# Optimization experiments

Measured on AMD Instinct MI355X. Metric: run time of the kernel, lower is better.

## Reference

```python
import jax, jax.numpy as jnp
import numpy as np

LENGTH_MIN = 5
LENGTH_MAX = 64
EMBED_DIM = 512
POOL_SIZE = 20
TOP_K = 5
BETA = 0.5
LN_EPS = 1e-5
COS_EPS = 1e-8


def setup_inputs() -> dict:
    key = jax.random.key(0)
    ks = jax.random.split(key, 8)
    B, N = 1024, 64
    H = EMBED_DIM // 2
    # xavier-uniform-ish init scale for params
    def xavier(k, shape, fan_in, fan_out):
        lim = float(np.sqrt(6.0 / (fan_in + fan_out)))
        return jax.random.uniform(k, shape, jnp.float32, -lim, lim)
    return {
        "x_embed": jax.random.normal(ks[0], (B, N, EMBED_DIM), jnp.float32),
        "quality_score": jax.random.uniform(ks[1], (B, 1), jnp.float32),
        "prompt_keys": xavier(ks[2], (POOL_SIZE, EMBED_DIM), POOL_SIZE, EMBED_DIM),
        "prompt_embeddings": xavier(ks[3], (POOL_SIZE, LENGTH_MAX, EMBED_DIM), LENGTH_MAX, EMBED_DIM),
        "w1": xavier(ks[4], (1, H), 1, H),
        "b1": jnp.zeros((H,), jnp.float32),
        "ln_g": jnp.ones((H,), jnp.float32),
        "ln_b": jnp.zeros((H,), jnp.float32),
        "w2": xavier(ks[5], (H, EMBED_DIM), H, EMBED_DIM),
        "b2": jnp.zeros((EMBED_DIM,), jnp.float32),
    }


def _quality_proj(q, w1, b1, ln_g, ln_b, w2, b2):
    h = q @ w1 + b1  # [B, H]
    mu = h.mean(-1, keepdims=True)
    var = ((h - mu) ** 2).mean(-1, keepdims=True)
    h = (h - mu) * jax.lax.rsqrt(var + LN_EPS) * ln_g + ln_b
    h = jax.nn.relu(h)
    return h @ w2 + b2  # [B, D]


def reference(x_embed, quality_score, prompt_keys, prompt_embeddings, w1, b1, ln_g, ln_b, w2, b2):
    query = _quality_proj(quality_score, w1, b1, ln_g, ln_b, w2, b2)  # [B, D]
    # cosine similarity vs pool keys
    qn = query / jnp.maximum(jnp.linalg.norm(query, axis=-1, keepdims=True), COS_EPS)
    kn = prompt_keys / jnp.maximum(jnp.linalg.norm(prompt_keys, axis=-1, keepdims=True), COS_EPS)
    sims = qn @ kn.T  # [B, P]
    scale = 1.0 + BETA * quality_score.mean()
    weights = jax.nn.softmax(sims * scale, axis=1)  # [B, P]
    # batched top-k (replaces the per-sample Python loop)
    topk_w, topk_idx = jax.lax.top_k(weights, TOP_K)  # [B, K]
    # per-sample dynamic length -> validity mask over length_max positions
    mu_b = quality_score.mean(axis=1)  # [B]; quality_score[b:b+1].mean()
    len_f = LENGTH_MIN + (LENGTH_MAX - LENGTH_MIN) * (1.0 - mu_b / 5.0)
    lens = jnp.clip(jnp.trunc(len_f).astype(jnp.int32), LENGTH_MIN, LENGTH_MAX)  # [B]
    mask = (jnp.arange(LENGTH_MAX)[None, :] < lens[:, None]).astype(x_embed.dtype)  # [B, L]
    # gather selected prompts and weighted-sum over top_k
    sel = prompt_embeddings[topk_idx]  # [B, K, L, D]
    out = jnp.einsum("bk,bkld->bld", topk_w, sel) * mask[:, :, None]  # [B, L, D]
    return out
```

## Files before the change

kernel.cpp:

```cpp
#include <hip/hip_runtime.h>
#include <hip/hip_bf16.h>
#include <math.h>

#define LENGTH_MIN 5
#define LENGTH_MAX 64
#define EMBED_DIM 512
#define HDIM      256
#define POOL      20
#define TOPK      5
#define BETA      0.5f
#define LN_EPS    1e-5f
#define COS_EPS   1e-8f


__device__ __forceinline__ float blockReduceSum(float v, float* red) {
    int t = threadIdx.x;
    red[t] = v;
    __syncthreads();
    for (int off = 128; off > 0; off >>= 1) {
        if (t < off) red[t] += red[t + off];
        __syncthreads();
    }
    float r = red[0];
    __syncthreads();
    return r;
}

__global__ __launch_bounds__(256) void prep_kernel(
    const float* __restrict__ quality, const float* __restrict__ keys,
    const float* __restrict__ w1, const float* __restrict__ b1,
    float* __restrict__ ws, int B)
{
    __shared__ float red[256];
    int t = threadIdx.x;
    int blk = blockIdx.x;
    if (blk == 0) {
        float s = 0.f;
        for (int i = t; i < B; i += 256) s += quality[i];
        float tot = blockReduceSum(s, red);
        if (t == 0) ws[0] = tot / (float)B;
    } else if (blk == 1) {
        float a = w1[t];
        float c = b1[t];
        float mw1 = blockReduceSum(a, red) / 256.f;
        float mb1 = blockReduceSum(c, red) / 256.f;
        float da = a - mw1, dc = c - mb1;
        float Vw1 = blockReduceSum(da * da, red) / 256.f;
        float Vb1 = blockReduceSum(dc * dc, red) / 256.f;
        float Cv  = blockReduceSum(da * dc, red) / 256.f;
        if (t == 0) { ws[1] = mw1; ws[2] = mb1; ws[3] = Vw1; ws[4] = Vb1; ws[5] = Cv; }
    } else {
        int p = blk - 2;
        const float* kp = keys + p * EMBED_DIM;
        float s = 0.f;
        float x0 = kp[t], x1 = kp[t + 256];
        s = x0 * x0 + x1 * x1;
        float n2 = blockReduceSum(s, red);
        if (t == 0) ws[8 + p] = 1.f / fmaxf(sqrtf(n2), COS_EPS);
    }
}

__global__ __launch_bounds__(256) void query_kernel(
    const float* __restrict__ quality, const float* __restrict__ keys,
    const float* __restrict__ w1, const float* __restrict__ b1,
    const float* __restrict__ ln_g, const float* __restrict__ ln_b,
    const float* __restrict__ w2, const float* __restrict__ b2,
    float* __restrict__ ws, int B)
{
    __shared__ float hn_s[4][HDIM];
    __shared__ float qbuf[4][EMBED_DIM];
    int t = threadIdx.x;
    int b0 = blockIdx.x * 4;

    float qmean = ws[0];
    float mw1 = ws[1], mb1 = ws[2], Vw1 = ws[3], Vb1 = ws[4], Cv = ws[5];
    float invk[POOL];
    #pragma unroll
    for (int p = 0; p < POOL; p++) invk[p] = ws[8 + p];

    float w1t = w1[t], b1t = b1[t], gt = ln_g[t], lbt = ln_b[t];
    float qv4[4];
    #pragma unroll
    for (int bi = 0; bi < 4; bi++) {
        float q = quality[b0 + bi];
        qv4[bi] = q;
        float mu  = q * mw1 + mb1;
        float var = q * q * Vw1 + 2.f * q * Cv + Vb1;
        float inv = rsqrtf(var + LN_EPS);
        float h = q * w1t + b1t;
        float v = (h - mu) * inv * gt + lbt;
        hn_s[bi][t] = fmaxf(v, 0.f);
    }
    __syncthreads();

    int d0 = 2 * t;
    float2 b2v = *(const float2*)(b2 + d0);
    float acc0[4], acc1[4];
    #pragma unroll
    for (int bi = 0; bi < 4; bi++) { acc0[bi] = b2v.x; acc1[bi] = b2v.y; }

    for (int j = 0; j < HDIM; j += 4) {
        float2 wv0 = *(const float2*)(w2 + (j + 0) * EMBED_DIM + d0);
        float2 wv1 = *(const float2*)(w2 + (j + 1) * EMBED_DIM + d0);
        float2 wv2 = *(const float2*)(w2 + (j + 2) * EMBED_DIM + d0);
        float2 wv3 = *(const float2*)(w2 + (j + 3) * EMBED_DIM + d0);
        #pragma unroll
        for (int bi = 0; bi < 4; bi++) {
            float4 hv = *(const float4*)&hn_s[bi][j];
            acc0[bi] = fmaf(hv.x, wv0.x, acc0[bi]);
            acc1[bi] = fmaf(hv.x, wv0.y, acc1[bi]);
            acc0[bi] = fmaf(hv.y, wv1.x, acc0[bi]);
            acc1[bi] = fmaf(hv.y, wv1.y, acc1[bi]);
            acc0[bi] = fmaf(hv.z, wv2.x, acc0[bi]);
            acc1[bi] = fmaf(hv.z, wv2.y, acc1[bi]);
            acc0[bi] = fmaf(hv.w, wv3.x, acc0[bi]);
            acc1[bi] = fmaf(hv.w, wv3.y, acc1[bi]);
        }
    }
    #pragma unroll
    for (int bi = 0; bi < 4; bi++) {
        *(float2*)&qbuf[bi][d0] = make_float2(acc0[bi], acc1[bi]);
    }
    __syncthreads();

    int wave = t >> 6, lane = t & 63;
    int bi = wave;
    float s[POOL + 1];
    #pragma unroll
    for (int p = 0; p <= POOL; p++) s[p] = 0.f;
    #pragma unroll
    for (int i = 0; i < 8; i++) {
        int d = lane + 64 * i;
        float qd = qbuf[bi][d];
        s[POOL] = fmaf(qd, qd, s[POOL]);
        #pragma unroll
        for (int p = 0; p < POOL; p++)
            s[p] = fmaf(qd, keys[p * EMBED_DIM + d], s[p]);
    }
    #pragma unroll
    for (int off = 32; off > 0; off >>= 1) {
        #pragma unroll
        for (int p = 0; p <= POOL; p++) s[p] += __shfl_xor(s[p], off);
    }

    float invq = 1.f / fmaxf(sqrtf(s[POOL]), COS_EPS);
    float scale = 1.f + BETA * qmean;
    float sim[POOL];
    #pragma unroll
    for (int p = 0; p < POOL; p++) sim[p] = s[p] * invq * invk[p] * scale;

    float m = sim[0];
    #pragma unroll
    for (int p = 1; p < POOL; p++) m = fmaxf(m, sim[p]);
    float e[POOL]; float den = 0.f;
    #pragma unroll
    for (int p = 0; p < POOL; p++) { e[p] = __expf(sim[p] - m); den += e[p]; }
    den = 0.f;
    #pragma unroll
    for (int p = 0; p < POOL; p++) { e[p] = expf(sim[p] - m); den += e[p]; }
    float invden = 1.f / den;

    unsigned picked = 0;
    float tw[TOPK]; int ti[TOPK];
    #pragma unroll
    for (int k = 0; k < TOPK; k++) {
        float best = -1.f; int bidx = 0;
        #pragma unroll
        for (int p = 0; p < POOL; p++) {
            bool free_p = ((picked >> p) & 1u) == 0u;
            if (free_p && e[p] > best) { best = e[p]; bidx = p; }
        }
        picked |= (1u << bidx);
        tw[k] = best * invden;
        ti[k] = bidx;
    }

    if (lane == 0) {
        int b = b0 + bi;
        float* topw = ws + 32;
        int*   topi = (int*)(ws + 32) + 5 * B;
        int*   lenp = (int*)(ws + 32) + 10 * B;
        #pragma unroll
        for (int k = 0; k < TOPK; k++) {
            topw[b * TOPK + k] = tw[k];
            topi[b * TOPK + k] = ti[k];
        }
        float q = qv4[bi];
        float lf = __fadd_rn(5.f, __fmul_rn(59.f, __fsub_rn(1.f, __fdiv_rn(q, 5.f))));
        int len = (int)truncf(lf);
        len = min(max(len, LENGTH_MIN), LENGTH_MAX);
        lenp[b] = len;
    }
}

__global__ __launch_bounds__(256) void scatter_kernel(
    const float* __restrict__ pe, const float* __restrict__ ws,
    float* __restrict__ out, int B)
{
    int b  = blockIdx.x >> 3;
    int l0 = (blockIdx.x & 7) * 8;
    const float* topw = ws + 32;
    const int*   topi = (const int*)(ws + 32) + 5 * B;
    const int*   lenp = (const int*)(ws + 32) + 10 * B;

    float w[TOPK]; int idx[TOPK];
    #pragma unroll
    for (int k = 0; k < TOPK; k++) {
        w[k]   = topw[b * TOPK + k];
        idx[k] = topi[b * TOPK + k];
    }
    int len = lenp[b];

    int t = threadIdx.x;
    #pragma unroll
    for (int sweep = 0; sweep < 4; sweep++) {
        int l  = l0 + sweep * 2 + (t >> 7);
        int d4 = (t & 127) * 4;
        float4 r = make_float4(0.f, 0.f, 0.f, 0.f);
        if (l < len) {
            #pragma unroll
            for (int k = 0; k < TOPK; k++) {
                const float4 pv = *(const float4*)(pe + (idx[k] * 64 + l) * EMBED_DIM + d4);
                r.x = fmaf(w[k], pv.x, r.x);
                r.y = fmaf(w[k], pv.y, r.y);
                r.z = fmaf(w[k], pv.z, r.z);
                r.w = fmaf(w[k], pv.w, r.w);
            }
        }
        *(float4*)(out + ((size_t)(b * 64 + l)) * EMBED_DIM + d4) = r;
    }
}

extern "C" void kernel_launch(void* const* d_in, const int* in_sizes, int n_in,
                              void* d_out, int out_size, void* d_ws, size_t ws_size,
                              hipStream_t stream) {
    const float* quality = (const float*)d_in[1];
    const float* keys    = (const float*)d_in[2];
    const float* pe      = (const float*)d_in[3];
    const float* w1      = (const float*)d_in[4];
    const float* b1      = (const float*)d_in[5];
    const float* ln_g    = (const float*)d_in[6];
    const float* ln_b    = (const float*)d_in[7];
    const float* w2      = (const float*)d_in[8];
    const float* b2      = (const float*)d_in[9];
    float* out = (float*)d_out;
    float* ws  = (float*)d_ws;
    int B = in_sizes[1];

    prep_kernel<<<2 + POOL, 256, 0, stream>>>(quality, keys, w1, b1, ws, B);
    query_kernel<<<B / 4, 256, 0, stream>>>(quality, keys, w1, b1, ln_g, ln_b, w2, b2, ws, B);
    scatter_kernel<<<B * 8, 256, 0, stream>>>(pe, ws, out, B);
}
```

Measured before the change: 294.9 us.

## Fold prep stats into query kernel and use nontemporal output stores

```diff
diff --git a/kernel.cpp b/kernel.cpp
--- a/kernel.cpp
+++ b/kernel.cpp
@@ -12,73 +12,60 @@
 #define LN_EPS    1e-5f
 #define COS_EPS   1e-8f
 
-
-__device__ __forceinline__ float blockReduceSum(float v, float* red) {
-    int t = threadIdx.x;
-    red[t] = v;
-    __syncthreads();
-    for (int off = 128; off > 0; off >>= 1) {
-        if (t < off) red[t] += red[t + off];
-        __syncthreads();
-    }
-    float r = red[0];
-    __syncthreads();
-    return r;
-}
-
-__global__ __launch_bounds__(256) void prep_kernel(
-    const float* __restrict__ quality, const float* __restrict__ keys,
-    const float* __restrict__ w1, const float* __restrict__ b1,
-    float* __restrict__ ws, int B)
-{
-    __shared__ float red[256];
-    int t = threadIdx.x;
-    int blk = blockIdx.x;
-    if (blk == 0) {
-        float s = 0.f;
-        for (int i = t; i < B; i += 256) s += quality[i];
-        float tot = blockReduceSum(s, red);
-        if (t == 0) ws[0] = tot / (float)B;
-    } else if (blk == 1) {
-        float a = w1[t];
-        float c = b1[t];
-        float mw1 = blockReduceSum(a, red) / 256.f;
-        float mb1 = blockReduceSum(c, red) / 256.f;
-        float da = a - mw1, dc = c - mb1;
-        float Vw1 = blockReduceSum(da * da, red) / 256.f;
-        float Vb1 = blockReduceSum(dc * dc, red) / 256.f;
-        float Cv  = blockReduceSum(da * dc, red) / 256.f;
-        if (t == 0) { ws[1] = mw1; ws[2] = mb1; ws[3] = Vw1; ws[4] = Vb1; ws[5] = Cv; }
-    } else {
-        int p = blk - 2;
-        const float* kp = keys + p * EMBED_DIM;
-        float s = 0.f;
-        float x0 = kp[t], x1 = kp[t + 256];
-        s = x0 * x0 + x1 * x1;
-        float n2 = blockReduceSum(s, red);
-        if (t == 0) ws[8 + p] = 1.f / fmaxf(sqrtf(n2), COS_EPS);
-    }
-}
-
-__global__ __launch_bounds__(256) void query_kernel(
+typedef float v4f __attribute__((ext_vector_type(4)));
+
+
+__global__ __launch_bounds__(256) void query_all_kernel(
     const float* __restrict__ quality, const float* __restrict__ keys,
     const float* __restrict__ w1, const float* __restrict__ b1,
     const float* __restrict__ ln_g, const float* __restrict__ ln_b,
     const float* __restrict__ w2, const float* __restrict__ b2,
     float* __restrict__ ws, int B)
 {
+    __shared__ float red[24];
+    __shared__ float invk_s[POOL];
     __shared__ float hn_s[4][HDIM];
     __shared__ float qbuf[4][EMBED_DIM];
+
     int t = threadIdx.x;
+    int wave = t >> 6, lane = t & 63;
     int b0 = blockIdx.x * 4;
 
-    float qmean = ws[0];
-    float mw1 = ws[1], mb1 = ws[2], Vw1 = ws[3], Vb1 = ws[4], Cv = ws[5];
-    float invk[POOL];
-    #pragma unroll
-    for (int p = 0; p < POOL; p++) invk[p] = ws[8 + p];
-
-    float w1t = w1[t], b1t = b1[t], gt = ln_g[t], lbt = ln_b[t];
+    float qpart = 0.f;
+    for (int i = t; i < B; i += 256) qpart += quality[i];
+    float a = w1[t], c = b1[t];
+    float vals[6] = { qpart, a, a * a, c, c * c, a * c };
+    #pragma unroll
+    for (int i = 0; i < 6; i++) {
+        float v = vals[i];
+        #pragma unroll
+        for (int off = 32; off > 0; off >>= 1) v += __shfl_xor(v, off);
+        if (lane == 0) red[i * 4 + wave] = v;
+    }
+    #pragma unroll
+    for (int j = 0; j < 5; j++) {
+        int p = wave + 4 * j;
+        const float* kp = keys + p * EMBED_DIM;
+        float s = 0.f;
+        #pragma unroll
+        for (int i = 0; i < 8; i++) { float x = kp[lane + 64 * i]; s = fmaf(x, x, s); }
+        #pragma unroll
+        for (int off = 32; off > 0; off >>= 1) s += __shfl_xor(s, off);
+        if (lane == 0) invk_s[p] = 1.f / fmaxf(sqrtf(s), COS_EPS);
+    }
+    __syncthreads();
+
+    float qmean = (red[0] + red[1] + red[2] + red[3]) / (float)B;
+    float mw1   = (red[4] + red[5] + red[6] + red[7]) * (1.f / 256.f);
+    float Ew2   = (red[8] + red[9] + red[10] + red[11]) * (1.f / 256.f);
+    float mb1   = (red[12] + red[13] + red[14] + red[15]) * (1.f / 256.f);
+    float Eb2   = (red[16] + red[17] + red[18] + red[19]) * (1.f / 256.f);
+    float Eab   = (red[20] + red[21] + red[22] + red[23]) * (1.f / 256.f);
+    float Vw1 = Ew2 - mw1 * mw1;
+    float Vb1 = Eb2 - mb1 * mb1;
+    float Cv  = Eab - mw1 * mb1;
+
+    float gt = ln_g[t], lbt = ln_b[t];
     float qv4[4];
     #pragma unroll
     for (int bi = 0; bi < 4; bi++) {
@@ -87,9 +74,8 @@
         float mu  = q * mw1 + mb1;
         float var = q * q * Vw1 + 2.f * q * Cv + Vb1;
         float inv = rsqrtf(var + LN_EPS);
-        float h = q * w1t + b1t;
-        float v = (h - mu) * inv * gt + lbt;
-        hn_s[bi][t] = fmaxf(v, 0.f);
+        float h = q * a + c;
+        hn_s[bi][t] = fmaxf((h - mu) * inv * gt + lbt, 0.f);
     }
     __syncthreads();
 
@@ -118,12 +104,10 @@
         }
     }
     #pragma unroll
-    for (int bi = 0; bi < 4; bi++) {
+    for (int bi = 0; bi < 4; bi++)
         *(float2*)&qbuf[bi][d0] = make_float2(acc0[bi], acc1[bi]);
-    }
     __syncthreads();
 
-    int wave = t >> 6, lane = t & 63;
     int bi = wave;
     float s[POOL + 1];
     #pragma unroll
@@ -143,19 +127,16 @@
         for (int p = 0; p <= POOL; p++) s[p] += __shfl_xor(s[p], off);
     }
 
-    float invq = 1.f / fmaxf(sqrtf(s[POOL]), COS_EPS);
+    float invq  = 1.f / fmaxf(sqrtf(s[POOL]), COS_EPS);
     float scale = 1.f + BETA * qmean;
     float sim[POOL];
     #pragma unroll
-    for (int p = 0; p < POOL; p++) sim[p] = s[p] * invq * invk[p] * scale;
+    for (int p = 0; p < POOL; p++) sim[p] = s[p] * invq * invk_s[p] * scale;
 
     float m = sim[0];
     #pragma unroll
     for (int p = 1; p < POOL; p++) m = fmaxf(m, sim[p]);
     float e[POOL]; float den = 0.f;
-    #pragma unroll
-    for (int p = 0; p < POOL; p++) { e[p] = __expf(sim[p] - m); den += e[p]; }
-    den = 0.f;
     #pragma unroll
     for (int p = 0; p < POOL; p++) { e[p] = expf(sim[p] - m); den += e[p]; }
     float invden = 1.f / den;
@@ -216,18 +197,15 @@
     for (int sweep = 0; sweep < 4; sweep++) {
         int l  = l0 + sweep * 2 + (t >> 7);
         int d4 = (t & 127) * 4;
-        float4 r = make_float4(0.f, 0.f, 0.f, 0.f);
+        v4f r = { 0.f, 0.f, 0.f, 0.f };
         if (l < len) {
             #pragma unroll
             for (int k = 0; k < TOPK; k++) {
-                const float4 pv = *(const float4*)(pe + (idx[k] * 64 + l) * EMBED_DIM + d4);
-                r.x = fmaf(w[k], pv.x, r.x);
-                r.y = fmaf(w[k], pv.y, r.y);
-                r.z = fmaf(w[k], pv.z, r.z);
-                r.w = fmaf(w[k], pv.w, r.w);
+                v4f pv = *(const v4f*)(pe + (idx[k] * 64 + l) * EMBED_DIM + d4);
+                r += pv * w[k];
             }
         }
-        *(float4*)(out + ((size_t)(b * 64 + l)) * EMBED_DIM + d4) = r;
+        __builtin_nontemporal_store(r, (v4f*)(out + ((size_t)(b * 64 + l)) * EMBED_DIM + d4));
     }
 }
 
@@ -247,7 +225,7 @@
     float* ws  = (float*)d_ws;
     int B = in_sizes[1];
 
-    prep_kernel<<<2 + POOL, 256, 0, stream>>>(quality, keys, w1, b1, ws, B);
-    query_kernel<<<B / 4, 256, 0, stream>>>(quality, keys, w1, b1, ln_g, ln_b, w2, b2, ws, B);
+    query_all_kernel<<<B / 4, 256, 0, stream>>>(quality, keys, w1, b1, ln_g, ln_b,
+                                                w2, b2, ws, B);
     scatter_kernel<<<B * 8, 256, 0, stream>>>(pe, ws, out, B);
 }
```

Result: faster. 274.2 us (-7.0%).
